# Performance work log

Measured on AMD Instinct MI355X. Metric: run time of the kernel, lower is better.

Reference implementation:

```python
import jax, jax.numpy as jnp
import numpy as np
from jax import lax

DN3D = ('NDHWC', 'DHWIO', 'NDHWC')


def _conv3d(x, w):
    return lax.conv_general_dilated(x, w, window_strides=(1, 1, 1),
                                    padding='VALID', dimension_numbers=DN3D)


def _cconv3d(xr, xi, wr, wi):
    # (xr + i xi) * (wr + i wi)
    yr = _conv3d(xr, wr) - _conv3d(xi, wi)
    yi = _conv3d(xr, wi) + _conv3d(xi, wr)
    return yr, yi


def _project(wr, wi, zero_mean):
    # zero-mean + bound-norm weight projection over (kD,kH,kW,Cin) per output filter
    ax = (0, 1, 2, 3)
    if zero_mean:
        wr = wr - jnp.mean(wr, ax, keepdims=True)
        wi = wi - jnp.mean(wi, ax, keepdims=True)
    norm = jnp.sqrt(jnp.sum(wr * wr + wi * wi, ax, keepdims=True))
    s = 1.0 / jnp.maximum(norm, 1.0)
    return wr * s, wi * s


def _sympad(x, pads):
    # pads: list of (lo, hi) per axis
    return jnp.pad(x, pads, mode='symmetric')


def setup_inputs() -> dict:
    key = jax.random.key(0)
    ks = jax.random.split(key, 6)
    B, T, Z, Y, X, C = 2, 8, 20, 64, 64, 2
    F1, F = 32, 32
    return {
        'xr': jax.random.normal(ks[0], (B, T, Z, Y, X, C), jnp.float32),
        'xi': jax.random.normal(ks[1], (B, T, Z, Y, X, C), jnp.float32),
        'wxyz_r': jax.random.normal(ks[2], (3, 3, 3, C, F1), jnp.float32) * 0.1,
        'wxyz_i': jax.random.normal(ks[3], (3, 3, 3, C, F1), jnp.float32) * 0.1,
        'wt_r': jax.random.normal(ks[4], (3, 1, 1, F1, F), jnp.float32) * 0.1,
        'wt_i': jax.random.normal(ks[5], (3, 1, 1, F1, F), jnp.float32) * 0.1,
    }


def reference(xr, xi, wxyz_r, wxyz_i, wt_r, wt_i):
    B, T, Z, Y, X, C = xr.shape
    kz, ky, kx = wxyz_r.shape[0], wxyz_r.shape[1], wxyz_r.shape[2]
    kt = wt_r.shape[0]
    F1 = wxyz_r.shape[-1]
    F = wt_r.shape[-1]

    # projected (zero-mean, bound-norm) complex kernels
    wsr, wsi = _project(wxyz_r, wxyz_i, zero_mean=True)
    wtr, wti = _project(wt_r, wt_i, zero_mean=False)

    # --- spatial 3D conv over (Z,Y,X): fold T into batch (== per-T-slice loop)
    sr = xr.reshape(B * T, Z, Y, X, C)
    si = xi.reshape(B * T, Z, Y, X, C)
    pads_sp = [(0, 0), (kz // 2, kz // 2), (ky // 2, ky // 2), (kx // 2, kx // 2), (0, 0)]
    sr = _sympad(sr, pads_sp)
    si = _sympad(si, pads_sp)
    spr, spi = _cconv3d(sr, si, wsr, wsi)          # [B*T, Z, Y, X, F1]
    spr = spr.reshape(B, T, Z, Y, X, F1)
    spi = spi.reshape(B, T, Z, Y, X, F1)

    # --- temporal conv (kt,1,1) over (T,Z,Y): fold X into batch (== per-X-slice loop)
    tr = spr.transpose(0, 4, 1, 2, 3, 5).reshape(B * X, T, Z, Y, F1)
    ti = spi.transpose(0, 4, 1, 2, 3, 5).reshape(B * X, T, Z, Y, F1)
    pads_t = [(0, 0), (kt // 2, kt // 2), (0, 0), (0, 0), (0, 0)]
    tr = _sympad(tr, pads_t)
    ti = _sympad(ti, pads_t)
    ytr, yti = _cconv3d(tr, ti, wtr, wti)          # [B*X, T, Z, Y, F]
    yr = ytr.reshape(B, X, T, Z, Y, F).transpose(0, 2, 3, 4, 1, 5)
    yi = yti.reshape(B, X, T, Z, Y, F).transpose(0, 2, 3, 4, 1, 5)
    return yr, yi
```

## Files before the change

### kernel.cpp

```cpp
#include <hip/hip_runtime.h>

#define B_ 2
#define T_ 8
#define Z_ 20
#define Y_ 64
#define X_ 64
#define C_ 2
#define F1_ 32
#define F_ 32

constexpr int NPTS = B_*T_*Z_*Y_*X_;
constexpr int ZYX  = Z_*Y_*X_;

constexpr int RING_STRIDE = 36;
constexpr int SLOT_DW     = 16*RING_STRIDE;

using bf8   = __attribute__((ext_vector_type(8))) short;
using f32x4 = __attribute__((ext_vector_type(4))) float;

__device__ inline unsigned short f2bf(float x) {
    unsigned u = __builtin_bit_cast(unsigned, x);
    return (unsigned short)((u + 0x7fff + ((u >> 16) & 1)) >> 16);
}

__global__ __launch_bounds__(64) void project_kernel(
    const float* __restrict__ wxr, const float* __restrict__ wxi,
    const float* __restrict__ wtr, const float* __restrict__ wti,
    float* __restrict__ psr, float* __restrict__ psi,
    float* __restrict__ otr, float* __restrict__ oti)
{
    const int bid  = blockIdx.x;
    const int lane = threadIdx.x;

    if (bid < F1_) {
        const int f = bid;
        float er = 0.f, ei = 0.f;
        if (lane < 54) { er = wxr[lane*F1_ + f]; ei = wxi[lane*F1_ + f]; }
        float sr = er, si = ei;
        #pragma unroll
        for (int o = 32; o >= 1; o >>= 1) { sr += __shfl_xor(sr, o); si += __shfl_xor(si, o); }
        const float mr = sr * (1.f/54.f), mi = si * (1.f/54.f);
        const float dr = er - mr, di = ei - mi;
        float sq = (lane < 54) ? (dr*dr + di*di) : 0.f;
        #pragma unroll
        for (int o = 32; o >= 1; o >>= 1) sq += __shfl_xor(sq, o);
        const float s = 1.f / fmaxf(sqrtf(sq), 1.f);
        if (lane < 54) { psr[lane*F1_ + f] = dr*s; psi[lane*F1_ + f] = di*s; }
    } else {
        const int f = bid - F1_;
        float er[2], ei[2];
        float sq = 0.f;
        #pragma unroll
        for (int k = 0; k < 2; ++k) {
            const int e = lane + k*64;
            if (e < 96) { er[k] = wtr[e*F_ + f]; ei[k] = wti[e*F_ + f]; sq += er[k]*er[k] + ei[k]*ei[k]; }
            else        { er[k] = 0.f;  ei[k] = 0.f; }
        }
        #pragma unroll
        for (int o = 32; o >= 1; o >>= 1) sq += __shfl_xor(sq, o);
        const float s = 1.f / fmaxf(sqrtf(sq), 1.f);
        #pragma unroll
        for (int k = 0; k < 2; ++k) {
            const int e = lane + k*64;
            if (e < 96) { otr[e*F_ + f] = er[k]*s; oti[e*F_ + f] = ei[k]*s; }
        }
    }
}

__global__ __launch_bounds__(256) void pack_kernel(
    const float* __restrict__ psr, const float* __restrict__ psi,
    const float* __restrict__ ptr_, const float* __restrict__ pti,
    unsigned short* __restrict__ wsp, unsigned short* __restrict__ wp)
{
    const int g = blockIdx.x;
    if (g < 16) {
        for (int o = g*512 + threadIdx.x; o < (g+1)*512; o += 256) {
            const int j  = o & 7;
            const int l  = (o >> 3) & 63;
            const int gg = o >> 9;
            const int kb = gg & 3, ct = gg >> 2;
            const int k  = kb*32 + (l >> 4)*8 + j;
            const int n  = ct*16 + (l & 15);
            float v = 0.f;
            if (k < 108) {
                const int tap = k >> 2, q = k & 3, cin = q & 1, cp = q >> 1;
                const int f  = n & 31;
                const float wr = psr[(tap*2 + cin)*F1_ + f];
                const float wi = psi[(tap*2 + cin)*F1_ + f];
                v = (n < 32) ? (cp ? -wi : wr) : (cp ? wr : wi);
            }
            wsp[o] = f2bf(v);
        }
    } else {
        for (int o = (g-16)*512 + threadIdx.x; o < (g-15)*512; o += 256) {
            const int j  = o & 7;
            const int l  = (o >> 3) & 63;
            const int gg = o >> 9;
            const int kb = gg % 6, ct = gg / 6;
            const int k  = kb*32 + (l >> 4)*8 + j;
            const int n  = ct*16 + (l & 15);
            const int kt = k >> 6, f1 = (k >> 1) & 31, c = k & 1;
            const int f  = n & 31;
            const float wr = ptr_[(kt*F1_ + f1)*F_ + f];
            const float wi = pti[(kt*F1_ + f1)*F_ + f];
            const float v  = (n < 32) ? (c ? -wi : wr) : (c ? wr : wi);
            wp[o] = f2bf(v);
        }
    }
}

__global__ __launch_bounds__(256) void repack_kernel(
    const float* __restrict__ xr, const float* __restrict__ xi,
    uint2* __restrict__ xb)
{
    const int p = blockIdx.x*256 + threadIdx.x;
    const float2 vr = *reinterpret_cast<const float2*>(xr + (size_t)p*2);
    const float2 vi = *reinterpret_cast<const float2*>(xi + (size_t)p*2);
    uint2 v;
    v.x = (unsigned)f2bf(vr.x) | ((unsigned)f2bf(vr.y) << 16);
    v.y = (unsigned)f2bf(vi.x) | ((unsigned)f2bf(vi.y) << 16);
    xb[p] = v;
}

__global__ __launch_bounds__(256) void fused_kernel(
    const uint2* __restrict__ xb,
    const unsigned short* __restrict__ wsp,
    const unsigned short* __restrict__ wp,
    float* __restrict__ yr, float* __restrict__ yi)
{
    __shared__ unsigned ring[4*3*SLOT_DW];

    const int tid  = threadIdx.x;
    const int lane = tid & 63;
    const int wid  = tid >> 6;
    const int lx   = lane & 15;
    const int lg   = lane >> 4;

    const int bq = blockIdx.x;
    const int y  = bq & 63;
    const int z  = (bq >> 6) % Z_;
    const int b  = bq / (64*Z_);
    const int x0 = wid * 16;

    bf8 wsf[4][4];
    const bf8* w8 = reinterpret_cast<const bf8*>(wsp);
    #pragma unroll
    for (int ct = 0; ct < 4; ++ct)
        #pragma unroll
        for (int kb = 0; kb < 4; ++kb)
            wsf[ct][kb] = w8[(ct*4 + kb)*64 + lane];

    bf8 wtf[4][6];
    const bf8* wp8 = reinterpret_cast<const bf8*>(wp);
    #pragma unroll
    for (int ct = 0; ct < 4; ++ct)
        #pragma unroll
        for (int kb = 0; kb < 6; ++kb)
            wtf[ct][kb] = wp8[(ct*6 + kb)*64 + lane];

    int off[4][2];
    #pragma unroll
    for (int kb = 0; kb < 4; ++kb)
        #pragma unroll
        for (int s = 0; s < 2; ++s) {
            int ta = kb*8 + lg*2 + s; if (ta > 26) ta = 26;
            const int dz = ta/9, dyx = ta - dz*9, dy = dyx/3, dx = dyx - dy*3;
            int zz = z + dz - 1;      zz = zz < 0 ? 0 : (zz >= Z_ ? Z_-1 : zz);
            int yy = y + dy - 1;      yy = yy < 0 ? 0 : (yy >= Y_ ? Y_-1 : yy);
            int xx = x0 + lx + dx - 1; xx = xx < 0 ? 0 : (xx >= X_ ? X_-1 : xx);
            off[kb][s] = (zz*Y_ + yy)*X_ + xx;
        }

    unsigned* myring = ring + wid*3*SLOT_DW;
    const size_t yrow_base = (((size_t)b*T_)*Z_ + z)*Y_*X_ + (size_t)y*X_ + x0 + lg*4;

    auto EMIT = [&](int sa, int sb, int sc, int tout) {
        const int sl[3] = {sa % 3, sb % 3, sc % 3};
        bf8 af[6];
        #pragma unroll
        for (int kt = 0; kt < 3; ++kt) {
            const unsigned* base = myring + sl[kt]*SLOT_DW + lx*RING_STRIDE + lg*4;
            const uint4 u0 = *reinterpret_cast<const uint4*>(base);
            const uint4 u1 = *reinterpret_cast<const uint4*>(base + 16);
            af[kt*2+0] = __builtin_bit_cast(bf8, u0);
            af[kt*2+1] = __builtin_bit_cast(bf8, u1);
        }
        f32x4 acc[4];
        #pragma unroll
        for (int ct = 0; ct < 4; ++ct) acc[ct] = (f32x4){0.f,0.f,0.f,0.f};
        #pragma unroll
        for (int ct = 0; ct < 4; ++ct)
            #pragma unroll
            for (int kb = 0; kb < 6; ++kb)
                acc[ct] = __builtin_amdgcn_mfma_f32_16x16x32_bf16(
                              af[kb], wtf[ct][kb], acc[ct], 0, 0, 0);
        const size_t prow = yrow_base + (size_t)tout * ZYX;
        #pragma unroll
        for (int ct = 0; ct < 4; ++ct) {
            float* outp = (ct < 2) ? yr : yi;
            const int f = (ct & 1)*16 + lx;
            #pragma unroll
            for (int j = 0; j < 4; ++j)
                outp[(prow + j)*F_ + f] = acc[ct][j];
        }
    };

    #pragma unroll 1
    for (int t = 0; t < T_; ++t) {
        const uint2* xt = xb + (size_t)(b*T_ + t)*ZYX;
        bf8 af[4];
        #pragma unroll
        for (int kb = 0; kb < 4; ++kb) {
            const uint2 lo = xt[off[kb][0]];
            const uint2 hi = xt[off[kb][1]];
            af[kb] = __builtin_bit_cast(bf8, make_uint4(lo.x, lo.y, hi.x, hi.y));
        }
        f32x4 acc[4];
        #pragma unroll
        for (int ct = 0; ct < 4; ++ct) acc[ct] = (f32x4){0.f,0.f,0.f,0.f};
        #pragma unroll
        for (int ct = 0; ct < 4; ++ct)
            #pragma unroll
            for (int kb = 0; kb < 4; ++kb)
                acc[ct] = __builtin_amdgcn_mfma_f32_16x16x32_bf16(
                              af[kb], wsf[ct][kb], acc[ct], 0, 0, 0);

        unsigned* slot = myring + (t % 3)*SLOT_DW;
        #pragma unroll
        for (int j = 0; j < 4; ++j) {
            const unsigned v0 = (unsigned)f2bf(acc[0][j]) | ((unsigned)f2bf(acc[2][j]) << 16);
            const unsigned v1 = (unsigned)f2bf(acc[1][j]) | ((unsigned)f2bf(acc[3][j]) << 16);
            unsigned* row = slot + (lg*4 + j)*RING_STRIDE;
            row[lx]      = v0;
            row[16 + lx] = v1;
        }

        if (t >= 1) EMIT(t-2 < 0 ? 0 : t-2, t-1, t, t-1);
    }
    EMIT(T_-2, T_-1, T_-1, T_-1);
}

extern "C" void kernel_launch(void* const* d_in, const int* in_sizes, int n_in,
                              void* d_out, int out_size, void* d_ws, size_t ws_size,
                              hipStream_t stream)
{
    const float* xr  = (const float*)d_in[0];
    const float* xi  = (const float*)d_in[1];
    const float* wxr = (const float*)d_in[2];
    const float* wxi = (const float*)d_in[3];
    const float* wtr = (const float*)d_in[4];
    const float* wti = (const float*)d_in[5];

    float* ws   = (float*)d_ws;
    float* psr  = ws;
    float* psi  = ws + 2048;
    float* ptr_ = ws + 4096;
    float* pti  = ws + 8192;
    unsigned short* wsp = (unsigned short*)(ws + 12288);
    unsigned short* wp  = (unsigned short*)(ws + 16384);
    uint2* xb           = (uint2*)(ws + 32768);

    float* yr = (float*)d_out;
    float* yi = yr + (size_t)NPTS * F_;

    hipLaunchKernelGGL(project_kernel, dim3(64), dim3(64), 0, stream,
                       wxr, wxi, wtr, wti, psr, psi, ptr_, pti);
    hipLaunchKernelGGL(pack_kernel, dim3(40), dim3(256), 0, stream,
                       psr, psi, ptr_, pti, wsp, wp);
    hipLaunchKernelGGL(repack_kernel, dim3(NPTS/256), dim3(256), 0, stream,
                       xr, xi, xb);
    hipLaunchKernelGGL(fused_kernel, dim3(B_*Z_*Y_), dim3(256), 0, stream,
                       xb, wsp, wp, yr, yi);
}
```

Baseline: 101.9 us.

## Keep spatial conv results in registers via transposed MFMA, drop LDS ring

Swaps the MFMA operand order so the spatial conv output lands in registers already laid out as the B operand of the temporal MFMA. That removes the shared-memory ring buffer and its writes and reads between the two stages. The time loop is fully unrolled with a register rotation of three slots. Output stores become 16-byte vector stores of four consecutive filters instead of scalar strided stores. Register pressure rises, and the unrolled code is larger.

```diff
diff --git a/kernel.cpp b/kernel.cpp
--- a/kernel.cpp
+++ b/kernel.cpp
@@ -12,15 +12,15 @@
 constexpr int NPTS = B_*T_*Z_*Y_*X_;
 constexpr int ZYX  = Z_*Y_*X_;
 
-constexpr int RING_STRIDE = 36;
-constexpr int SLOT_DW     = 16*RING_STRIDE;
-
 using bf8   = __attribute__((ext_vector_type(8))) short;
 using f32x4 = __attribute__((ext_vector_type(4))) float;
 
 __device__ inline unsigned short f2bf(float x) {
     unsigned u = __builtin_bit_cast(unsigned, x);
     return (unsigned short)((u + 0x7fff + ((u >> 16) & 1)) >> 16);
+}
+__device__ inline unsigned pk(float a, float b) {
+    return (unsigned)f2bf(a) | ((unsigned)f2bf(b) << 16);
 }
 
 __global__ __launch_bounds__(64) void project_kernel(
@@ -128,8 +128,6 @@
     const unsigned short* __restrict__ wp,
     float* __restrict__ yr, float* __restrict__ yi)
 {
-    __shared__ unsigned ring[4*3*SLOT_DW];
-
     const int tid  = threadIdx.x;
     const int lane = tid & 63;
     const int wid  = tid >> 6;
@@ -171,20 +169,41 @@
             off[kb][s] = (zz*Y_ + yy)*X_ + xx;
         }
 
-    unsigned* myring = ring + wid*3*SLOT_DW;
-    const size_t yrow_base = (((size_t)b*T_)*Z_ + z)*Y_*X_ + (size_t)y*X_ + x0 + lg*4;
-
-    auto EMIT = [&](int sa, int sb, int sc, int tout) {
-        const int sl[3] = {sa % 3, sb % 3, sc % 3};
-        bf8 af[6];
-        #pragma unroll
-        for (int kt = 0; kt < 3; ++kt) {
-            const unsigned* base = myring + sl[kt]*SLOT_DW + lx*RING_STRIDE + lg*4;
-            const uint4 u0 = *reinterpret_cast<const uint4*>(base);
-            const uint4 u1 = *reinterpret_cast<const uint4*>(base + 16);
-            af[kt*2+0] = __builtin_bit_cast(bf8, u0);
-            af[kt*2+1] = __builtin_bit_cast(bf8, u1);
-        }
+    const size_t orow = (((size_t)b*T_)*Z_ + z)*(size_t)(Y_*X_) + (size_t)y*X_ + x0 + lx;
+
+    uint4 sl_lo[3], sl_hi[3];
+
+    auto SPATIAL = [&](int t, uint4& lo, uint4& hi) {
+        const uint2* xt = xb + (size_t)(b*T_ + t)*ZYX;
+        bf8 af[4];
+        #pragma unroll
+        for (int kb = 0; kb < 4; ++kb) {
+            const uint2 l2 = xt[off[kb][0]];
+            const uint2 h2 = xt[off[kb][1]];
+            af[kb] = __builtin_bit_cast(bf8, make_uint4(l2.x, l2.y, h2.x, h2.y));
+        }
+        f32x4 acc[4];
+        #pragma unroll
+        for (int ct = 0; ct < 4; ++ct) acc[ct] = (f32x4){0.f,0.f,0.f,0.f};
+        #pragma unroll
+        for (int ct = 0; ct < 4; ++ct)
+            #pragma unroll
+            for (int kb = 0; kb < 4; ++kb)
+                acc[ct] = __builtin_amdgcn_mfma_f32_16x16x32_bf16(
+                              wsf[ct][kb], af[kb], acc[ct], 0, 0, 0);
+        lo = make_uint4(pk(acc[0][0],acc[2][0]), pk(acc[0][1],acc[2][1]),
+                        pk(acc[0][2],acc[2][2]), pk(acc[0][3],acc[2][3]));
+        hi = make_uint4(pk(acc[1][0],acc[3][0]), pk(acc[1][1],acc[3][1]),
+                        pk(acc[1][2],acc[3][2]), pk(acc[1][3],acc[3][3]));
+    };
+
+    auto EMIT = [&](const uint4& alo, const uint4& ahi,
+                    const uint4& blo, const uint4& bhi,
+                    const uint4& clo, const uint4& chi, int tout) {
+        bf8 fr[6];
+        fr[0] = __builtin_bit_cast(bf8, alo); fr[1] = __builtin_bit_cast(bf8, ahi);
+        fr[2] = __builtin_bit_cast(bf8, blo); fr[3] = __builtin_bit_cast(bf8, bhi);
+        fr[4] = __builtin_bit_cast(bf8, clo); fr[5] = __builtin_bit_cast(bf8, chi);
         f32x4 acc[4];
         #pragma unroll
         for (int ct = 0; ct < 4; ++ct) acc[ct] = (f32x4){0.f,0.f,0.f,0.f};
@@ -193,51 +212,31 @@
             #pragma unroll
             for (int kb = 0; kb < 6; ++kb)
                 acc[ct] = __builtin_amdgcn_mfma_f32_16x16x32_bf16(
-                              af[kb], wtf[ct][kb], acc[ct], 0, 0, 0);
-        const size_t prow = yrow_base + (size_t)tout * ZYX;
+                              wtf[ct][kb], fr[kb], acc[ct], 0, 0, 0);
+        const size_t p = orow + (size_t)tout * ZYX;
         #pragma unroll
         for (int ct = 0; ct < 4; ++ct) {
             float* outp = (ct < 2) ? yr : yi;
-            const int f = (ct & 1)*16 + lx;
-            #pragma unroll
-            for (int j = 0; j < 4; ++j)
-                outp[(prow + j)*F_ + f] = acc[ct][j];
+            *reinterpret_cast<f32x4*>(outp + p*F_ + (ct & 1)*16 + lg*4) = acc[ct];
         }
     };
 
-    #pragma unroll 1
-    for (int t = 0; t < T_; ++t) {
-        const uint2* xt = xb + (size_t)(b*T_ + t)*ZYX;
-        bf8 af[4];
-        #pragma unroll
-        for (int kb = 0; kb < 4; ++kb) {
-            const uint2 lo = xt[off[kb][0]];
-            const uint2 hi = xt[off[kb][1]];
-            af[kb] = __builtin_bit_cast(bf8, make_uint4(lo.x, lo.y, hi.x, hi.y));
-        }
-        f32x4 acc[4];
-        #pragma unroll
-        for (int ct = 0; ct < 4; ++ct) acc[ct] = (f32x4){0.f,0.f,0.f,0.f};
-        #pragma unroll
-        for (int ct = 0; ct < 4; ++ct)
-            #pragma unroll
-            for (int kb = 0; kb < 4; ++kb)
-                acc[ct] = __builtin_amdgcn_mfma_f32_16x16x32_bf16(
-                              af[kb], wsf[ct][kb], acc[ct], 0, 0, 0);
-
-        unsigned* slot = myring + (t % 3)*SLOT_DW;
-        #pragma unroll
-        for (int j = 0; j < 4; ++j) {
-            const unsigned v0 = (unsigned)f2bf(acc[0][j]) | ((unsigned)f2bf(acc[2][j]) << 16);
-            const unsigned v1 = (unsigned)f2bf(acc[1][j]) | ((unsigned)f2bf(acc[3][j]) << 16);
-            unsigned* row = slot + (lg*4 + j)*RING_STRIDE;
-            row[lx]      = v0;
-            row[16 + lx] = v1;
-        }
-
-        if (t >= 1) EMIT(t-2 < 0 ? 0 : t-2, t-1, t, t-1);
-    }
-    EMIT(T_-2, T_-1, T_-1, T_-1);
+    SPATIAL(0, sl_lo[0], sl_hi[0]);
+    SPATIAL(1, sl_lo[1], sl_hi[1]);
+    EMIT(sl_lo[0],sl_hi[0], sl_lo[0],sl_hi[0], sl_lo[1],sl_hi[1], 0);
+    SPATIAL(2, sl_lo[2], sl_hi[2]);
+    EMIT(sl_lo[0],sl_hi[0], sl_lo[1],sl_hi[1], sl_lo[2],sl_hi[2], 1);
+    SPATIAL(3, sl_lo[0], sl_hi[0]);
+    EMIT(sl_lo[1],sl_hi[1], sl_lo[2],sl_hi[2], sl_lo[0],sl_hi[0], 2);
+    SPATIAL(4, sl_lo[1], sl_hi[1]);
+    EMIT(sl_lo[2],sl_hi[2], sl_lo[0],sl_hi[0], sl_lo[1],sl_hi[1], 3);
+    SPATIAL(5, sl_lo[2], sl_hi[2]);
+    EMIT(sl_lo[0],sl_hi[0], sl_lo[1],sl_hi[1], sl_lo[2],sl_hi[2], 4);
+    SPATIAL(6, sl_lo[0], sl_hi[0]);
+    EMIT(sl_lo[1],sl_hi[1], sl_lo[2],sl_hi[2], sl_lo[0],sl_hi[0], 5);
+    SPATIAL(7, sl_lo[1], sl_hi[1]);
+    EMIT(sl_lo[2],sl_hi[2], sl_lo[0],sl_hi[0], sl_lo[1],sl_hi[1], 6);
+    EMIT(sl_lo[0],sl_hi[0], sl_lo[1],sl_hi[1], sl_lo[1],sl_hi[1], 7);
 }
 
 extern "C" void kernel_launch(void* const* d_in, const int* in_sizes, int n_in,
```

New measurement: 129.3 us. 1.27x slower.
